# Kernel tuning notes

Measured on AMD Instinct MI355X. Metric: run time of the kernel, lower is better.

## Reference

```python
import jax, jax.numpy as jnp
import numpy as np
import math
from jax import lax

WINDOWS = (3, 5, 7)
GRIDSIZE = 3
HALF_H = 384  # hidden of each directional LSTM (d_model // 2)


def _lstm_last(x, mask, Wih, Whh, bih, bhh, reverse):
    """Masked single-layer LSTM; returns final hidden state.
    x: [N, T, D], mask: [N, T] bool. Invalid steps leave (h, c) unchanged,
    which is equivalent to running the LSTM only over the valid contiguous
    sub-window (leading/trailing pads are skipped).
    PyTorch gate order: i, f, g, o.
    """
    N = x.shape[0]
    H = Whh.shape[1]
    h0 = jnp.zeros((N, H), x.dtype)
    c0 = jnp.zeros((N, H), x.dtype)

    def step(carry, inp):
        h, c = carry
        xt, mt = inp
        gates = xt @ Wih.T + h @ Whh.T + (bih + bhh)
        i, f, g, o = jnp.split(gates, 4, axis=-1)
        i = jax.nn.sigmoid(i); f = jax.nn.sigmoid(f); o = jax.nn.sigmoid(o)
        g = jnp.tanh(g)
        c_new = f * c + i * g
        h_new = o * jnp.tanh(c_new)
        m = mt[:, None]
        return (jnp.where(m, h_new, h), jnp.where(m, c_new, c)), None

    xs = (jnp.moveaxis(x, 1, 0), jnp.moveaxis(mask, 1, 0))
    (h, _), _ = lax.scan(step, (h0, c0), xs, reverse=reverse)
    return h


def setup_inputs() -> dict:
    key = jax.random.key(0)
    ks = jax.random.split(key, 12)
    B, L, D = 16, 512, 768
    H4 = 4 * HALF_H
    s = 0.02
    inp = {
        'sequence_output': jax.random.normal(ks[0], (B, L, D), jnp.float32),
        'Wih_f': jax.random.normal(ks[1], (3, H4, D), jnp.float32) * s,
        'Whh_f': jax.random.normal(ks[2], (3, H4, HALF_H), jnp.float32) * s,
        'bih_f': jax.random.normal(ks[3], (3, H4), jnp.float32) * s,
        'bhh_f': jax.random.normal(ks[4], (3, H4), jnp.float32) * s,
        'Wih_b': jax.random.normal(ks[5], (3, H4, D), jnp.float32) * s,
        'Whh_b': jax.random.normal(ks[6], (3, H4, HALF_H), jnp.float32) * s,
        'bih_b': jax.random.normal(ks[7], (3, H4), jnp.float32) * s,
        'bhh_b': jax.random.normal(ks[8], (3, H4), jnp.float32) * s,
        'kan_coeffs': jax.random.normal(ks[9], (2, 11, GRIDSIZE, D), jnp.float32)
                      / (np.sqrt(D) * np.sqrt(GRIDSIZE)),
        'kan_bias': jax.random.normal(ks[10], (11,), jnp.float32) * s,
        'valid_ids': jax.random.randint(ks[11], (B, L), 0, 2, jnp.int64),
    }
    return inp


def reference(sequence_output, Wih_f, Whh_f, bih_f, bhh_f,
              Wih_b, Whh_b, bih_b, bhh_b, kan_coeffs, kan_bias, valid_ids):
    B, L, D = sequence_output.shape
    # ---- valid-id compaction (scatter valid tokens to the front, zeros after)
    v = valid_ids == 1
    dest = jnp.where(v, jnp.cumsum(v, axis=1) - 1, L)  # invalid -> dump slot L
    bidx = jnp.arange(B)[:, None]
    valid_output = (jnp.zeros((B, L + 1, D), sequence_output.dtype)
                    .at[bidx, dest].set(sequence_output))[:, :L]
    x = valid_output  # dropout is identity in eval

    # ---- per-window sliding BiLSTM (vectorized over all B*L positions)
    outs = []
    for wi, w in enumerate(WINDOWS):
        half = w // 2
        idx = jnp.arange(L)[:, None] + jnp.arange(-half, half + 1)[None, :]  # [L,w]
        valid = (idx >= 0) & (idx < L)
        idxc = jnp.clip(idx, 0, L - 1)
        xw = x[:, idxc].reshape(B * L, w, D)                  # [B*L, w, D]
        m = jnp.broadcast_to(valid[None], (B, L, w)).reshape(B * L, w)
        hf = _lstm_last(xw, m, Wih_f[wi], Whh_f[wi], bih_f[wi], bhh_f[wi], False)
        hb = _lstm_last(xw, m, Wih_b[wi], Whh_b[wi], bih_b[wi], bhh_b[wi], True)
        outs.append(jnp.concatenate([hf, hb], axis=-1).reshape(B, L, D))

    seq = outs[0] + outs[1] + outs[2]

    # ---- 'dot-att' fusion over window features
    stk = jnp.stack(outs, axis=2)                             # [B, L, K, D]
    q = seq[:, :, None, :]                                    # [B, L, 1, D]
    attn = jax.nn.softmax(
        jnp.einsum('blqd,blkd->blqk', q, stk) / math.sqrt(D), axis=-1)
    local = jnp.einsum('blqk,blkd->blqd', attn, stk)[:, :, 0]
    seq = seq + local

    # ---- NaiveFourierKAN classifier (gridsize=3)
    k = jnp.arange(1, GRIDSIZE + 1, dtype=seq.dtype)
    xg = seq[..., None, :] * k[:, None]                       # [B, L, g, D]
    logits = (jnp.einsum('blgi,ogi->blo', jnp.cos(xg), kan_coeffs[0])
              + jnp.einsum('blgi,ogi->blo', jnp.sin(xg), kan_coeffs[1])
              + kan_bias)
    return logits
```

## Files before the change

### kernel.cpp

```cpp
#include <hip/hip_runtime.h>

#define BT 8192
#define SEQL 512
#define DIM 768
#define HID 384
#define NG 1536

using US = unsigned short;
typedef __bf16 bf16x8 __attribute__((ext_vector_type(8)));
typedef float f32x4 __attribute__((ext_vector_type(4)));

__device__ __forceinline__ float b2f(US u) {
  union { unsigned u; float f; } x; x.u = ((unsigned)u) << 16; return x.f;
}
__device__ __forceinline__ US f2b(float f) {
  __bf16 h = (__bf16)f;
  union { __bf16 h; US u; } x; x.h = h; return x.u;
}
__device__ __forceinline__ float fsig(float x) { return 1.f / (1.f + __expf(-x)); }
__device__ __forceinline__ float ftanh(float x) { return 1.f - 2.f / (__expf(2.f * x) + 1.f); }

__device__ __forceinline__ size_t pk_off(int panel, int rloc, int col, int panelStride) {
  return (size_t)panel * panelStride + (col >> 6) * 8192 + ((col >> 5) & 1) * 4096 +
         (rloc >> 6) * 2048 + ((rloc >> 4) & 3) * 512 +
         (((rloc & 15) | (((col & 31) >> 3) << 4))) * 8 + (col & 7);
}

__global__ __launch_bounds__(256) void convW_ih_k(const float* __restrict__ WihF,
                                                  const float* __restrict__ WihB,
                                                  US* __restrict__ WihP) {
  int d = blockIdx.z;
  const float* src = d ? WihB : WihF;
  size_t idx = (size_t)blockIdx.x * 256 + threadIdx.x;
  int lane = (int)(idx & 63);
  int t = (int)(idx >> 6);
  int sg = t & 3;
  int wn = (t >> 2) & 1;
  int kk = (t >> 3) & 1;
  int kt = (t >> 4) % 12;
  int nb = (t / 192) % 12;
  int wi = t / (192 * 12);
  int srow = sg * HID + nb * 32 + wn * 16 + (lane & 15);
  int scol = kt * 64 + kk * 32 + (lane >> 4) * 8;
  const float* s = src + ((size_t)wi * NG + srow) * DIM + scol;
  float4 v0 = *(const float4*)s;
  float4 v1 = *(const float4*)(s + 4);
  ushort4 o0, o1;
  o0.x = f2b(v0.x); o0.y = f2b(v0.y); o0.z = f2b(v0.z); o0.w = f2b(v0.w);
  o1.x = f2b(v1.x); o1.y = f2b(v1.y); o1.z = f2b(v1.z); o1.w = f2b(v1.w);
  US* dst = WihP + ((size_t)d * 442368 + idx) * 8;
  *(ushort4*)dst = o0;
  *(ushort4*)(dst + 4) = o1;
}

__global__ __launch_bounds__(256) void convW_hh_k(const float* __restrict__ WhhF,
                                                  const float* __restrict__ WhhB,
                                                  US* __restrict__ WhhP) {
  int d = blockIdx.z;
  const float* src = d ? WhhB : WhhF;
  size_t idx = (size_t)blockIdx.x * 256 + threadIdx.x;
  int lane = (int)(idx & 63);
  int t = (int)(idx >> 6);
  int sg = t & 3;
  int wn = (t >> 2) & 1;
  int kk = (t >> 3) & 1;
  int kt = (t >> 4) % 6;
  int hb = (t / 96) % 12;
  int wi = t / (96 * 12);
  int srow = sg * HID + hb * 32 + wn * 16 + (lane & 15);
  int scol = kt * 64 + kk * 32 + (lane >> 4) * 8;
  const float* s = src + ((size_t)wi * NG + srow) * HID + scol;
  float4 v0 = *(const float4*)s;
  float4 v1 = *(const float4*)(s + 4);
  ushort4 o0, o1;
  o0.x = f2b(v0.x); o0.y = f2b(v0.y); o0.z = f2b(v0.z); o0.w = f2b(v0.w);
  o1.x = f2b(v1.x); o1.y = f2b(v1.y); o1.z = f2b(v1.z); o1.w = f2b(v1.w);
  US* dst = WhhP + ((size_t)d * 221184 + idx) * 8;
  *(ushort4*)dst = o0;
  *(ushort4*)(dst + 4) = o1;
}

__global__ __launch_bounds__(256) void conv_coef_k(const float* __restrict__ coef,
                                                   US* __restrict__ coefP) {
  int idx = blockIdx.x * 256 + threadIdx.x;
  int s = idx & 31;
  int i = (idx >> 5) % DIM;
  int g = idx / (32 * DIM);
  float v = 0.f;
  int o = s & 15;
  if (o < 11) v = coef[(size_t)((s >> 4) * 33 + o * 3 + g) * DIM + i];
  coefP[idx] = f2b(v);
}

__global__ void scan_k(const int* __restrict__ valid, int* __restrict__ dest) {
  __shared__ int s[SEQL];
  int b = blockIdx.x, l = threadIdx.x;
  int v = (valid[b * SEQL + l] == 1) ? 1 : 0;
  s[l] = v;
  __syncthreads();
  for (int off = 1; off < SEQL; off <<= 1) {
    int t = (l >= off) ? s[l - off] : 0;
    __syncthreads();
    s[l] += t;
    __syncthreads();
  }
  dest[b * SEQL + l] = v ? (s[l] - 1) : -1;
}

__global__ __launch_bounds__(256) void scatter_k(const float* __restrict__ seq,
                                                 const int* __restrict__ dest,
                                                 US* __restrict__ xcP) {
  int idx = blockIdx.x * 256 + threadIdx.x;
  int p = idx / 192, cc = idx - p * 192;
  int d = dest[p];
  if (d < 0) return;
  int b = p >> 9;
  float4 v = ((const float4*)seq)[(size_t)p * 192 + cc];
  ushort4 o;
  o.x = f2b(v.x); o.y = f2b(v.y); o.z = f2b(v.z); o.w = f2b(v.w);
  int pdst = b * SEQL + d;
  int c = cc * 4;
  size_t off = pk_off(pdst >> 7, pdst & 127, c, 98304);
  *(ushort4*)&xcP[off] = o;
}

__global__ __launch_bounds__(256, 4) void gate_gemm_k(
    const US* __restrict__ xcP, const US* __restrict__ WihP,
    const float* __restrict__ bihF, const float* __restrict__ bihB,
    const float* __restrict__ bhhF, const float* __restrict__ bhhB,
    US* __restrict__ G, int dirBase, size_t gStr) {
  int zi = blockIdx.z;
  int wi = zi % 3, drz = zi / 3, dr = dirBase + drz;
  const float* bih = dr ? bihB : bihF;
  const float* bhh = dr ? bhhB : bhhF;
  int panel = blockIdx.x, nb = blockIdx.y;
  const US* Wp = WihP + ((size_t)(dr * 3 + wi) * 12 + nb) * 98304;
  US* Gw = G + (size_t)drz * gStr + (size_t)wi * BT * NG;
  __shared__ float biasS[128];
  int tid = threadIdx.x, lane = tid & 63, wid = tid >> 6;
  int wm = wid >> 1, wn = wid & 1;
  if (tid < 128) {
    int sg = tid >> 5, hl = tid & 31;
    int gc = wi * NG + sg * HID + nb * 32 + hl;
    biasS[tid] = bih[gc] + bhh[gc];
  }
  __syncthreads();
  f32x4 acc[4][4] = {};
  const US* Ab = xcP + (size_t)panel * 98304 + (size_t)wm * 2048 + (size_t)lane * 8;
  const US* Bb = Wp + (size_t)wn * 2048 + (size_t)lane * 8;
#pragma unroll 2
  for (int kp = 0; kp < 24; ++kp) {
    bf16x8 a[4], b[4];
    const US* ap = Ab + (size_t)kp * 4096;
    const US* bp = Bb + (size_t)kp * 4096;
#pragma unroll
    for (int mi = 0; mi < 4; ++mi) a[mi] = *(const bf16x8*)(ap + (size_t)mi * 512);
#pragma unroll
    for (int sg = 0; sg < 4; ++sg) b[sg] = *(const bf16x8*)(bp + (size_t)sg * 512);
#pragma unroll
    for (int mi = 0; mi < 4; ++mi)
#pragma unroll
      for (int sg = 0; sg < 4; ++sg)
        acc[mi][sg] = __builtin_amdgcn_mfma_f32_16x16x32_bf16(a[mi], b[sg], acc[mi][sg], 0, 0, 0);
  }
  int hh = wn * 16 + (lane & 15);
  int hidx = nb * 32 + hh;
  int m0 = panel * 128;
#pragma unroll
  for (int mi = 0; mi < 4; ++mi) {
#pragma unroll
    for (int r = 0; r < 4; ++r) {
      int p = m0 + wm * 64 + mi * 16 + ((lane >> 4) << 2) + r;
      ushort4 gv;
      gv.x = f2b(acc[mi][0][r] + biasS[hh]);
      gv.y = f2b(acc[mi][1][r] + biasS[32 + hh]);
      gv.z = f2b(acc[mi][2][r] + biasS[64 + hh]);
      gv.w = f2b(acc[mi][3][r] + biasS[96 + hh]);
      *(ushort4*)&Gw[(size_t)p * NG + (size_t)hidx * 4] = gv;
    }
  }
}

__global__ __launch_bounds__(384) void step0_k(const US* __restrict__ G, US* __restrict__ C,
                                               US* __restrict__ hn, int dirBase,
                                               size_t gStr, size_t cStr, size_t hStr) {
  int zi = blockIdx.z;
  int wi = zi % 3, drz = zi / 3, dr = dirBase + drz;
  int half = wi + 1;
  int dlt = dr ? half : -half;
  int p = blockIdx.x, hidx = threadIdx.x;
  int l = p & (SEQL - 1);
  const US* Gw = G + (size_t)drz * gStr + (size_t)wi * BT * NG;
  float c = 0.f, h = 0.f;
  int t = l + dlt;
  if ((unsigned)t < (unsigned)SEQL) {
    ushort4 gv = *(const ushort4*)&Gw[(size_t)(p + dlt) * NG + (size_t)hidx * 4];
    c = fsig(b2f(gv.x)) * ftanh(b2f(gv.z));
    h = fsig(b2f(gv.w)) * ftanh(c);
  }
  C[(size_t)drz * cStr + (size_t)wi * BT * HID + (size_t)p * HID + hidx] = f2b(c);
  hn[(size_t)drz * hStr + (size_t)wi * BT * HID + pk_off(p >> 7, p & 127, hidx, 49152)] = f2b(h);
}

__global__ __launch_bounds__(256, 4) void step_k(
    const US* __restrict__ WhhP,
    const US* __restrict__ G, US* __restrict__ C,
    const US* __restrict__ hcur, US* __restrict__ hnxt, US* __restrict__ Outs,
    int s, int wi0, int nact, int dirBase,
    size_t gStr, size_t cStr, size_t hStr) {
  int zi = blockIdx.z;
  int wi = wi0 + zi % nact, drz = zi / nact, dr = dirBase + drz;
  int w = 2 * wi + 3, half = wi + 1;
  int j = dr ? (w - 1 - s) : s;
  int dlt = j - half;
  bool fin = (s == w - 1);
  const US* Gw = G + (size_t)drz * gStr + (size_t)wi * BT * NG;
  US* Cw = C + (size_t)drz * cStr + (size_t)wi * BT * HID;
  const US* hc = hcur + (size_t)drz * hStr + (size_t)wi * BT * HID;
  US* hn = hnxt + (size_t)drz * hStr + (size_t)wi * BT * HID;
  US* Ow = Outs + (size_t)wi * BT * DIM + (dr ? HID : 0);
  int panel = blockIdx.x, hb = blockIdx.y;
  const US* Wp = WhhP + ((size_t)(dr * 3 + wi) * 12 + hb) * 49152;
  int tid = threadIdx.x, lane = tid & 63, wid = tid >> 6;
  int wm = wid >> 1, wn = wid & 1;
  f32x4 acc[4][4] = {};

  const US* Ab = hc + (size_t)panel * 49152 + (size_t)wm * 2048 + (size_t)lane * 8;
  const US* Bb = Wp + (size_t)wn * 2048 + (size_t)lane * 8;
#pragma unroll 2
  for (int kp = 0; kp < 12; ++kp) {
    bf16x8 a[4], b[4];
    const US* ap = Ab + (size_t)kp * 4096;
    const US* bp = Bb + (size_t)kp * 4096;
#pragma unroll
    for (int mi = 0; mi < 4; ++mi) a[mi] = *(const bf16x8*)(ap + (size_t)mi * 512);
#pragma unroll
    for (int sg = 0; sg < 4; ++sg) b[sg] = *(const bf16x8*)(bp + (size_t)sg * 512);
#pragma unroll
    for (int mi = 0; mi < 4; ++mi)
#pragma unroll
      for (int sg = 0; sg < 4; ++sg)
        acc[mi][sg] = __builtin_amdgcn_mfma_f32_16x16x32_bf16(a[mi], b[sg], acc[mi][sg], 0, 0, 0);
  }
  int l15 = lane & 15, l4 = lane >> 4;
  int hh = wn * 16 + l15;
  int hidx = hb * 32 + hh;
  int m0 = panel * 128;
  size_t wbase = (size_t)panel * 49152 + (size_t)hb * 4096 + (size_t)wm * 2048 +
                 (size_t)(wn * 2 + (l15 >> 3)) * 128 + (l15 & 7);
#pragma unroll
  for (int mi = 0; mi < 4; ++mi) {
#pragma unroll
    for (int r = 0; r < 4; ++r) {
      int p = m0 + wm * 64 + mi * 16 + (l4 << 2) + r;
      int l = p & (SEQL - 1);
      size_t po = wbase + (size_t)mi * 512 + (size_t)((l4 << 2) + r) * 8;
      float hval;
      if ((unsigned)(l + dlt) < (unsigned)SEQL) {
        ushort4 gv = *(const ushort4*)&Gw[(size_t)(p + dlt) * NG + (size_t)hidx * 4];
        float gi = acc[mi][0][r] + b2f(gv.x);
        float gf = acc[mi][1][r] + b2f(gv.y);
        float gg = acc[mi][2][r] + b2f(gv.z);
        float go = acc[mi][3][r] + b2f(gv.w);
        size_t ci = (size_t)p * HID + hidx;
        float c = fsig(gf) * b2f(Cw[ci]) + fsig(gi) * ftanh(gg);
        Cw[ci] = f2b(c);
        hval = fsig(go) * ftanh(c);
      } else {
        hval = b2f(hc[po]);
      }
      if (fin) Ow[(size_t)p * DIM + hidx] = f2b(hval);
      else hn[po] = f2b(hval);
    }
  }
}

#define RSTR 260
__global__ __launch_bounds__(256) void attn_kan_k(
    const US* __restrict__ Outs, const US* __restrict__ coefP,
    const float* __restrict__ kbias, float* __restrict__ out) {
  int p4 = blockIdx.x * 4;
  int tid = threadIdx.x, lane = tid & 63, wid = tid >> 6;
  __shared__ float lds[44 * RSTR];
  float sq[3][4];
  {
    float o0[3][4], o1[3][4], o2[3][4], q[3][4];
#pragma unroll
    for (int c = 0; c < 3; ++c) {
      int i = tid + 256 * c;
#pragma unroll
      for (int t = 0; t < 4; ++t) {
        o0[c][t] = b2f(Outs[(size_t)(p4 + t) * DIM + i]);
        o1[c][t] = b2f(Outs[(size_t)(BT + p4 + t) * DIM + i]);
        o2[c][t] = b2f(Outs[(size_t)(2 * BT + p4 + t) * DIM + i]);
        q[c][t] = o0[c][t] + o1[c][t] + o2[c][t];
      }
    }
    float d[3][4];
#pragma unroll
    for (int t = 0; t < 4; ++t) {
      d[0][t] = 0.f; d[1][t] = 0.f; d[2][t] = 0.f;
#pragma unroll
      for (int c = 0; c < 3; ++c) {
        d[0][t] += q[c][t] * o0[c][t];
        d[1][t] += q[c][t] * o1[c][t];
        d[2][t] += q[c][t] * o2[c][t];
      }
    }
#pragma unroll
    for (int off = 32; off; off >>= 1)
#pragma unroll
      for (int t = 0; t < 4; ++t) {
        d[0][t] += __shfl_down(d[0][t], off);
        d[1][t] += __shfl_down(d[1][t], off);
        d[2][t] += __shfl_down(d[2][t], off);
      }
    if (lane == 0)
#pragma unroll
      for (int t = 0; t < 4; ++t) {
        lds[(t * 3 + 0) * 4 + wid] = d[0][t];
        lds[(t * 3 + 1) * 4 + wid] = d[1][t];
        lds[(t * 3 + 2) * 4 + wid] = d[2][t];
      }
    __syncthreads();
    const float scl = 0.03608439182435161f;
#pragma unroll
    for (int t = 0; t < 4; ++t) {
      float s0 = (lds[(t * 3) * 4] + lds[(t * 3) * 4 + 1] + lds[(t * 3) * 4 + 2] + lds[(t * 3) * 4 + 3]) * scl;
      float s1 = (lds[(t * 3 + 1) * 4] + lds[(t * 3 + 1) * 4 + 1] + lds[(t * 3 + 1) * 4 + 2] + lds[(t * 3 + 1) * 4 + 3]) * scl;
      float s2 = (lds[(t * 3 + 2) * 4] + lds[(t * 3 + 2) * 4 + 1] + lds[(t * 3 + 2) * 4 + 2] + lds[(t * 3 + 2) * 4 + 3]) * scl;
      float mx = fmaxf(s0, fmaxf(s1, s2));
      float a0 = __expf(s0 - mx), a1 = __expf(s1 - mx), a2 = __expf(s2 - mx);
      float inv = 1.f / (a0 + a1 + a2);
      a0 *= inv; a1 *= inv; a2 *= inv;
#pragma unroll
      for (int c = 0; c < 3; ++c)
        sq[c][t] = q[c][t] + a0 * o0[c][t] + a1 * o1[c][t] + a2 * o2[c][t];
    }
  }
  float acc[11][4];
#pragma unroll
  for (int o = 0; o < 11; ++o)
#pragma unroll
    for (int t = 0; t < 4; ++t) acc[o][t] = 0.f;
#pragma unroll
  for (int c = 0; c < 3; ++c) {
    int i = tid + 256 * c;
#pragma unroll
    for (int g = 0; g < 3; ++g) {
      float sn[4], cs[4];
#pragma unroll
      for (int t = 0; t < 4; ++t) __sincosf(sq[c][t] * (float)(g + 1), &sn[t], &cs[t]);
      const US* cp = coefP + ((size_t)g * DIM + i) * 32;
      bf16x8 k0 = *(const bf16x8*)(cp);
      bf16x8 k1 = *(const bf16x8*)(cp + 8);
      bf16x8 k2 = *(const bf16x8*)(cp + 16);
      bf16x8 k3 = *(const bf16x8*)(cp + 24);
#pragma unroll
      for (int o = 0; o < 8; ++o) {
        float cc = (float)k0[o], ss = (float)k2[o];
#pragma unroll
        for (int t = 0; t < 4; ++t) acc[o][t] += cs[t] * cc + sn[t] * ss;
      }
#pragma unroll
      for (int o = 8; o < 11; ++o) {
        float cc = (float)k1[o - 8], ss = (float)k3[o - 8];
#pragma unroll
        for (int t = 0; t < 4; ++t) acc[o][t] += cs[t] * cc + sn[t] * ss;
      }
    }
  }
  __syncthreads();
#pragma unroll
  for (int o = 0; o < 11; ++o)
#pragma unroll
    for (int t = 0; t < 4; ++t)
      lds[(o * 4 + t) * RSTR + tid] = acc[o][t];
  __syncthreads();
  if (tid < 176) {
    int r = tid >> 2, qq = tid & 3;
    const float4* pv = (const float4*)&lds[r * RSTR + qq * 64];
    float4 s4 = pv[0];
#pragma unroll
    for (int k = 1; k < 16; ++k) {
      float4 v = pv[k];
      s4.x += v.x; s4.y += v.y; s4.z += v.z; s4.w += v.w;
    }
    float v = (s4.x + s4.y) + (s4.z + s4.w);
    v += __shfl_down(v, 1);
    v += __shfl_down(v, 2);
    if (qq == 0) {
      int o = r >> 2, t = r & 3;
      out[(size_t)(p4 + t) * 11 + o] = v + kbias[o];
    }
  }
}

extern "C" void kernel_launch(void* const* d_in, const int* in_sizes, int n_in,
                              void* d_out, int out_size, void* d_ws, size_t ws_size,
                              hipStream_t stream) {
  const float* seq = (const float*)d_in[0];
  const float* WihF = (const float*)d_in[1];
  const float* WhhF = (const float*)d_in[2];
  const float* bihF = (const float*)d_in[3];
  const float* bhhF = (const float*)d_in[4];
  const float* WihB = (const float*)d_in[5];
  const float* WhhB = (const float*)d_in[6];
  const float* bihB = (const float*)d_in[7];
  const float* bhhB = (const float*)d_in[8];
  const float* coef = (const float*)d_in[9];
  const float* kbias = (const float*)d_in[10];
  const int* valid = (const int*)d_in[11];

  constexpr size_t SZ_XC = (size_t)BT * DIM * 2;
  constexpr size_t SZ_DEST = (size_t)BT * 4;
  constexpr size_t SZ_CP = (size_t)3 * DIM * 32 * 2;
  constexpr size_t SZ_G1 = (size_t)3 * BT * NG * 2;
  constexpr size_t SZ_C1 = (size_t)3 * BT * HID * 2;
  constexpr size_t SZ_H1 = (size_t)3 * BT * HID * 2;
  constexpr size_t SZ_OUTS = (size_t)3 * BT * DIM * 2;
  constexpr size_t SZ_WIHP = (size_t)2 * 3 * NG * DIM * 2;
  constexpr size_t SZ_WHHP = (size_t)2 * 3 * NG * HID * 2;
  constexpr size_t GE = (size_t)3 * BT * NG;
  constexpr size_t CE = (size_t)3 * BT * HID;
  constexpr size_t HE = (size_t)3 * BT * HID;

  constexpr size_t NEED1 = SZ_XC + SZ_DEST + SZ_CP + SZ_WIHP + SZ_WHHP +
                           SZ_G1 + SZ_C1 + 2 * SZ_H1 + SZ_OUTS;
  constexpr size_t UNION = (SZ_XC + SZ_WIHP > SZ_OUTS) ? (SZ_XC + SZ_WIHP) : SZ_OUTS;
  constexpr size_t NEED2 = UNION + SZ_DEST + SZ_CP + SZ_WHHP +
                           2 * SZ_G1 + 2 * SZ_C1 + 4 * SZ_H1;
  if (ws_size < NEED1) return;
  const int ndir = (ws_size >= NEED2) ? 2 : 1;

  char* ws = (char*)d_ws;
  US *xcP, *coefP, *WihP, *WhhP, *G, *C, *h0, *h1, *Outs;
  int* dest;
  if (ndir == 2) {
    xcP = (US*)ws;
    WihP = (US*)(ws + SZ_XC);
    Outs = (US*)ws;
    char* p = ws + UNION;
    dest = (int*)p;                    p += SZ_DEST;
    coefP = (US*)p;                    p += SZ_CP;
    WhhP = (US*)p;                     p += SZ_WHHP;
    G = (US*)p;                        p += 2 * SZ_G1;
    C = (US*)p;                        p += 2 * SZ_C1;
    h0 = (US*)p;                       p += 2 * SZ_H1;
    h1 = (US*)p;
  } else {
    char* p = ws;
    xcP = (US*)p;                      p += SZ_XC;
    dest = (int*)p;                    p += SZ_DEST;
    coefP = (US*)p;                    p += SZ_CP;
    WihP = (US*)p;                     p += SZ_WIHP;
    WhhP = (US*)p;                     p += SZ_WHHP;
    G = (US*)p;                        p += SZ_G1;
    C = (US*)p;                        p += SZ_C1;
    h0 = (US*)p;                       p += SZ_H1;
    h1 = (US*)p;                       p += SZ_H1;
    Outs = (US*)p;
  }
  float* out = (float*)d_out;

  hipMemsetAsync(xcP, 0, SZ_XC, stream);
  scan_k<<<16, SEQL, 0, stream>>>(valid, dest);
  scatter_k<<<(BT * 192) / 256, 256, 0, stream>>>(seq, dest, xcP);
  conv_coef_k<<<288, 256, 0, stream>>>(coef, coefP);
  convW_ih_k<<<dim3(442368 / 256, 1, 2), 256, 0, stream>>>(WihF, WihB, WihP);
  convW_hh_k<<<dim3(221184 / 256, 1, 2), 256, 0, stream>>>(WhhF, WhhB, WhhP);

  if (ndir == 2) {
    gate_gemm_k<<<dim3(64, 12, 6), 256, 0, stream>>>(xcP, WihP, bihF, bihB, bhhF, bhhB,
                                                     G, 0, GE);
    step0_k<<<dim3(BT, 1, 6), HID, 0, stream>>>(G, C, h1, 0, GE, CE, HE);
    for (int s = 1; s < 7; ++s) {
      int nact = (s < 3) ? 3 : ((s < 5) ? 2 : 1);
      int wi0 = 3 - nact;
      US* hcur = (s & 1) ? h1 : h0;
      US* hnxt = (s & 1) ? h0 : h1;
      step_k<<<dim3(64, 12, nact * 2), 256, 0, stream>>>(WhhP, G, C, hcur, hnxt, Outs,
                                                         s, wi0, nact, 0, GE, CE, HE);
    }
  } else {
    for (int dir = 0; dir < 2; ++dir) {
      gate_gemm_k<<<dim3(64, 12, 3), 256, 0, stream>>>(xcP, WihP, bihF, bihB, bhhF, bhhB,
                                                       G, dir, 0);
      step0_k<<<dim3(BT, 1, 3), HID, 0, stream>>>(G, C, h1, dir, 0, 0, 0);
      for (int s = 1; s < 7; ++s) {
        int nact = (s < 3) ? 3 : ((s < 5) ? 2 : 1);
        int wi0 = 3 - nact;
        US* hcur = (s & 1) ? h1 : h0;
        US* hnxt = (s & 1) ? h0 : h1;
        step_k<<<dim3(64, 12, nact), 256, 0, stream>>>(WhhP, G, C, hcur, hnxt, Outs,
                                                       s, wi0, nact, dir, 0, 0, 0);
      }
    }
  }
  attn_kan_k<<<BT / 4, 256, 0, stream>>>(Outs, coefP, kbias, out);
}
```

Baseline: 764.9 us.

## Fuse LSTM step-0 into gate GEMM epilogue and prefetch gate loads in step kernel

The separate step0 kernel is removed. The gate GEMM epilogue now computes the first LSTM cell and hidden state directly from its fp32 accumulators and scatters them to the shifted positions, zeroing positions with no valid first step. This saves one launch and a full re-read of the gate buffer. The step kernel's epilogue is also restructured so the gate and cell-state loads for the next 16-row group are issued before the current group is processed. That software pipelining is meant to hide global-load latency, at the cost of more registers.

```diff
diff --git a/kernel.cpp b/kernel.cpp
--- a/kernel.cpp
+++ b/kernel.cpp
@@ -128,14 +128,19 @@
     const US* __restrict__ xcP, const US* __restrict__ WihP,
     const float* __restrict__ bihF, const float* __restrict__ bihB,
     const float* __restrict__ bhhF, const float* __restrict__ bhhB,
-    US* __restrict__ G, int dirBase, size_t gStr) {
+    US* __restrict__ G, US* __restrict__ C, US* __restrict__ h1,
+    int dirBase, size_t gStr, size_t cStr, size_t hStr) {
   int zi = blockIdx.z;
-  int wi = zi % 3, drz = zi / 3, dr = dirBase + drz;
+  int wi = zi % 3, drz = zi / 3, dr = dirBase + zi / 3;
   const float* bih = dr ? bihB : bihF;
   const float* bhh = dr ? bhhB : bhhF;
+  int half = wi + 1;
+  int dlt0 = dr ? half : -half;
   int panel = blockIdx.x, nb = blockIdx.y;
   const US* Wp = WihP + ((size_t)(dr * 3 + wi) * 12 + nb) * 98304;
   US* Gw = G + (size_t)drz * gStr + (size_t)wi * BT * NG;
+  US* Cw = C + (size_t)drz * cStr + (size_t)wi * BT * HID;
+  US* h1w = h1 + (size_t)drz * hStr + (size_t)wi * BT * HID;
   __shared__ float biasS[128];
   int tid = threadIdx.x, lane = tid & 63, wid = tid >> 6;
   int wm = wid >> 1, wn = wid & 1;
@@ -166,40 +171,35 @@
   int hh = wn * 16 + (lane & 15);
   int hidx = nb * 32 + hh;
   int m0 = panel * 128;
+  float b0 = biasS[hh], b1 = biasS[32 + hh], b2 = biasS[64 + hh], b3 = biasS[96 + hh];
 #pragma unroll
   for (int mi = 0; mi < 4; ++mi) {
 #pragma unroll
     for (int r = 0; r < 4; ++r) {
-      int p = m0 + wm * 64 + mi * 16 + ((lane >> 4) << 2) + r;
+      int q = m0 + wm * 64 + mi * 16 + ((lane >> 4) << 2) + r;
+      float gi = acc[mi][0][r] + b0;
+      float gf = acc[mi][1][r] + b1;
+      float gg = acc[mi][2][r] + b2;
+      float go = acc[mi][3][r] + b3;
       ushort4 gv;
-      gv.x = f2b(acc[mi][0][r] + biasS[hh]);
-      gv.y = f2b(acc[mi][1][r] + biasS[32 + hh]);
-      gv.z = f2b(acc[mi][2][r] + biasS[64 + hh]);
-      gv.w = f2b(acc[mi][3][r] + biasS[96 + hh]);
-      *(ushort4*)&Gw[(size_t)p * NG + (size_t)hidx * 4] = gv;
-    }
-  }
-}
-
-__global__ __launch_bounds__(384) void step0_k(const US* __restrict__ G, US* __restrict__ C,
-                                               US* __restrict__ hn, int dirBase,
-                                               size_t gStr, size_t cStr, size_t hStr) {
-  int zi = blockIdx.z;
-  int wi = zi % 3, drz = zi / 3, dr = dirBase + drz;
-  int half = wi + 1;
-  int dlt = dr ? half : -half;
-  int p = blockIdx.x, hidx = threadIdx.x;
-  int l = p & (SEQL - 1);
-  const US* Gw = G + (size_t)drz * gStr + (size_t)wi * BT * NG;
-  float c = 0.f, h = 0.f;
-  int t = l + dlt;
-  if ((unsigned)t < (unsigned)SEQL) {
-    ushort4 gv = *(const ushort4*)&Gw[(size_t)(p + dlt) * NG + (size_t)hidx * 4];
-    c = fsig(b2f(gv.x)) * ftanh(b2f(gv.z));
-    h = fsig(b2f(gv.w)) * ftanh(c);
-  }
-  C[(size_t)drz * cStr + (size_t)wi * BT * HID + (size_t)p * HID + hidx] = f2b(c);
-  hn[(size_t)drz * hStr + (size_t)wi * BT * HID + pk_off(p >> 7, p & 127, hidx, 49152)] = f2b(h);
+      gv.x = f2b(gi); gv.y = f2b(gf); gv.z = f2b(gg); gv.w = f2b(go);
+      *(ushort4*)&Gw[(size_t)q * NG + (size_t)hidx * 4] = gv;
+      int lq = q & (SEQL - 1);
+      int lp = lq - dlt0;
+      if (0 <= lp && lp < SEQL) {
+        int p0 = q - dlt0;
+        float c0 = fsig(gi) * ftanh(gg);
+        float h0 = fsig(go) * ftanh(c0);
+        Cw[(size_t)p0 * HID + hidx] = f2b(c0);
+        h1w[pk_off(p0 >> 7, p0 & 127, hidx, 49152)] = f2b(h0);
+      }
+      int lt = lq + dlt0;
+      if (!(0 <= lt && lt < SEQL)) {
+        Cw[(size_t)q * HID + hidx] = 0;
+        h1w[pk_off(q >> 7, q & 127, hidx, 49152)] = 0;
+      }
+    }
+  }
 }
 
 __global__ __launch_bounds__(256, 4) void step_k(
@@ -248,23 +248,40 @@
   int m0 = panel * 128;
   size_t wbase = (size_t)panel * 49152 + (size_t)hb * 4096 + (size_t)wm * 2048 +
                  (size_t)(wn * 2 + (l15 >> 3)) * 128 + (l15 & 7);
-#pragma unroll
-  for (int mi = 0; mi < 4; ++mi) {
+
+  auto loadg = [&](int mi, ushort4& g0, ushort4& g1, ushort4& g2, ushort4& g3,
+                   US& c0, US& c1, US& c2, US& c3) {
+    int pb = m0 + wm * 64 + mi * 16 + (l4 << 2);
+    int q0 = ((unsigned)((pb & (SEQL - 1)) + dlt) < (unsigned)SEQL) ? pb + dlt : pb;
+    int q1 = ((unsigned)(((pb + 1) & (SEQL - 1)) + dlt) < (unsigned)SEQL) ? pb + 1 + dlt : pb + 1;
+    int q2 = ((unsigned)(((pb + 2) & (SEQL - 1)) + dlt) < (unsigned)SEQL) ? pb + 2 + dlt : pb + 2;
+    int q3 = ((unsigned)(((pb + 3) & (SEQL - 1)) + dlt) < (unsigned)SEQL) ? pb + 3 + dlt : pb + 3;
+    g0 = *(const ushort4*)&Gw[(size_t)q0 * NG + (size_t)hidx * 4];
+    g1 = *(const ushort4*)&Gw[(size_t)q1 * NG + (size_t)hidx * 4];
+    g2 = *(const ushort4*)&Gw[(size_t)q2 * NG + (size_t)hidx * 4];
+    g3 = *(const ushort4*)&Gw[(size_t)q3 * NG + (size_t)hidx * 4];
+    c0 = Cw[(size_t)(pb    ) * HID + hidx];
+    c1 = Cw[(size_t)(pb + 1) * HID + hidx];
+    c2 = Cw[(size_t)(pb + 2) * HID + hidx];
+    c3 = Cw[(size_t)(pb + 3) * HID + hidx];
+  };
+  auto proc = [&](int mi, ushort4 g0, ushort4 g1, ushort4 g2, ushort4 g3,
+                  US c0, US c1, US c2, US c3) {
 #pragma unroll
     for (int r = 0; r < 4; ++r) {
+      ushort4 gvr = (r == 0) ? g0 : (r == 1) ? g1 : (r == 2) ? g2 : g3;
+      US cvr = (r == 0) ? c0 : (r == 1) ? c1 : (r == 2) ? c2 : c3;
       int p = m0 + wm * 64 + mi * 16 + (l4 << 2) + r;
       int l = p & (SEQL - 1);
       size_t po = wbase + (size_t)mi * 512 + (size_t)((l4 << 2) + r) * 8;
       float hval;
       if ((unsigned)(l + dlt) < (unsigned)SEQL) {
-        ushort4 gv = *(const ushort4*)&Gw[(size_t)(p + dlt) * NG + (size_t)hidx * 4];
-        float gi = acc[mi][0][r] + b2f(gv.x);
-        float gf = acc[mi][1][r] + b2f(gv.y);
-        float gg = acc[mi][2][r] + b2f(gv.z);
-        float go = acc[mi][3][r] + b2f(gv.w);
-        size_t ci = (size_t)p * HID + hidx;
-        float c = fsig(gf) * b2f(Cw[ci]) + fsig(gi) * ftanh(gg);
-        Cw[ci] = f2b(c);
+        float gi = acc[mi][0][r] + b2f(gvr.x);
+        float gf = acc[mi][1][r] + b2f(gvr.y);
+        float gg = acc[mi][2][r] + b2f(gvr.z);
+        float go = acc[mi][3][r] + b2f(gvr.w);
+        float c = fsig(gf) * b2f(cvr) + fsig(gi) * ftanh(gg);
+        Cw[(size_t)p * HID + hidx] = f2b(c);
         hval = fsig(go) * ftanh(c);
       } else {
         hval = b2f(hc[po]);
@@ -272,7 +289,18 @@
       if (fin) Ow[(size_t)p * DIM + hidx] = f2b(hval);
       else hn[po] = f2b(hval);
     }
-  }
+  };
+
+  ushort4 gA0, gA1, gA2, gA3, gB0, gB1, gB2, gB3;
+  US cA0, cA1, cA2, cA3, cB0, cB1, cB2, cB3;
+  loadg(0, gA0, gA1, gA2, gA3, cA0, cA1, cA2, cA3);
+  loadg(1, gB0, gB1, gB2, gB3, cB0, cB1, cB2, cB3);
+  proc(0, gA0, gA1, gA2, gA3, cA0, cA1, cA2, cA3);
+  loadg(2, gA0, gA1, gA2, gA3, cA0, cA1, cA2, cA3);
+  proc(1, gB0, gB1, gB2, gB3, cB0, cB1, cB2, cB3);
+  loadg(3, gB0, gB1, gB2, gB3, cB0, cB1, cB2, cB3);
+  proc(2, gA0, gA1, gA2, gA3, cA0, cA1, cA2, cA3);
+  proc(3, gB0, gB1, gB2, gB3, cB0, cB1, cB2, cB3);
 }
 
 #define RSTR 260
@@ -472,8 +500,7 @@
 
   if (ndir == 2) {
     gate_gemm_k<<<dim3(64, 12, 6), 256, 0, stream>>>(xcP, WihP, bihF, bihB, bhhF, bhhB,
-                                                     G, 0, GE);
-    step0_k<<<dim3(BT, 1, 6), HID, 0, stream>>>(G, C, h1, 0, GE, CE, HE);
+                                                     G, C, h1, 0, GE, CE, HE);
     for (int s = 1; s < 7; ++s) {
       int nact = (s < 3) ? 3 : ((s < 5) ? 2 : 1);
       int wi0 = 3 - nact;
@@ -485,8 +512,7 @@
   } else {
     for (int dir = 0; dir < 2; ++dir) {
       gate_gemm_k<<<dim3(64, 12, 3), 256, 0, stream>>>(xcP, WihP, bihF, bihB, bhhF, bhhB,
-                                                       G, dir, 0);
-      step0_k<<<dim3(BT, 1, 3), HID, 0, stream>>>(G, C, h1, dir, 0, 0, 0);
+                                                       G, C, h1, dir, 0, 0, 0);
       for (int s = 1; s < 7; ++s) {
         int nact = (s < 3) ? 3 : ((s < 5) ? 2 : 1);
         int wi0 = 3 - nact;
```

Result: no change. 775.2 us (+1.3%).
